# Optimization experiments

Hardware: AMD Instinct MI355X
Metric: run time of the kernel (lower is better)

Reference implementation:

```python
import jax, jax.numpy as jnp
import numpy as np

# ---- problem constants (match init_kwargs) ----
B, H, W = 8, 256, 256
GY, GX = 2 * H, 2 * W          # k_oversampling = 2
J = 7                          # interp_points
ALPHA = 2.34 * J               # Kaiser-Bessel shape parameter (torchkbnufft default)
N = 100000                     # number of non-uniform k-space samples


def _kb(u):
    """Kaiser-Bessel kernel, support |u| <= J/2 (numpy, setup-time only)."""
    arg = 1.0 - (2.0 * u / J) ** 2
    val = np.i0(ALPHA * np.sqrt(np.clip(arg, 0.0, None))) / np.i0(ALPHA)
    return np.where(np.abs(u) <= J / 2.0, val, 0.0)


def setup_inputs() -> dict:
    rng = np.random.default_rng(0)
    key = jax.random.key(0)

    # non-uniform frequencies in radians, shape (2, N) -- the stored uv plane
    uv = rng.uniform(-np.pi, np.pi, size=(2, N)).astype(np.float64)

    # ---- apodization (scaling) coefficients: 1 / FT{kb}((n - N/2)/G) per dim ----
    u = np.linspace(-J / 2.0, J / 2.0, 10001)
    du = u[1] - u[0]
    kbu = _kb(u)

    def scaling(n_im, n_grid):
        f = (np.arange(n_im) - n_im / 2.0) / n_grid          # image-domain freqs
        c = (kbu[None, :] * np.cos(2.0 * np.pi * f[:, None] * u[None, :])).sum(1) * du
        return (1.0 / c).astype(np.float32)

    sc_y = scaling(H, GY)
    sc_x = scaling(W, GX)

    # ---- precomputed interpolation matrix (indices + KB weights), per dim ----
    offs = np.arange(J) - J // 2                              # -3..3

    def interp(om, n_grid):
        t = (om * n_grid / (2.0 * np.pi)) % n_grid            # grid coords (N,)
        base = np.round(t)
        idx = (base[:, None] + offs[None, :]) % n_grid        # (N, J)
        wts = _kb(t[:, None] - (base[:, None] + offs[None, :]))
        return idx.astype(np.int32), wts.astype(np.float32)

    iy, wy = interp(uv[0], GY)
    ix, wx = interp(uv[1], GX)

    # centering phase: exp(1j * (om_y*H/2 + om_x*W/2)) for the n - N/2 convention
    ph = np.exp(1j * (uv[0] * H / 2.0 + uv[1] * W / 2.0))
    phr = ph.real.astype(np.float32)
    phi = ph.imag.astype(np.float32)

    k1, k2 = jax.random.split(key)
    xr = jax.random.normal(k1, (B, 1, H, W), dtype=jnp.float32)
    xi = jax.random.normal(k2, (B, 1, H, W), dtype=jnp.float32)

    return {
        "xr": xr, "xi": xi,
        "sc_y": jnp.asarray(sc_y), "sc_x": jnp.asarray(sc_x),
        "wy": jnp.asarray(wy), "wx": jnp.asarray(wx),
        "phr": jnp.asarray(phr), "phi": jnp.asarray(phi),
        "iy": jnp.asarray(iy), "ix": jnp.asarray(ix),
    }


def reference(xr, xi, sc_y, sc_x, wy, wx, phr, phi, iy, ix):
    """KB-NuFFT forward (dir_op): apodize -> oversampled ortho FFT -> KB gather.

    Returns (B, 1, N, 2) with real/imag of the k-space measurements.
    """
    b, c, h, w = xr.shape
    gy, gx = 2 * h, 2 * w

    # apodization correction then zero-pad to the oversampled grid
    x = (xr + 1j * xi) * (sc_y[:, None] * sc_x[None, :])      # (B,1,H,W) complex64
    xp = jnp.pad(x, ((0, 0), (0, 0), (0, gy - h), (0, gx - w)))
    ghat = jnp.fft.fft2(xp, norm="ortho")                      # (B,1,GY,GX)

    # sparse gather of the 7x7 neighborhood of every non-uniform point
    lin = (iy[:, :, None] * gx + ix[:, None, :]).reshape(-1)   # (N*J*J,)
    g = jnp.take(ghat.reshape(b, c, gy * gx), lin, axis=-1)
    g = g.reshape(b, c, -1, J, J)                              # (B,1,N,J,J)

    wgt = (wy[:, :, None] * wx[:, None, :]).astype(ghat.dtype)  # (N,J,J)
    k = jnp.einsum("bcnjk,njk->bcn", g, wgt)                   # (B,1,N) complex
    k = k * (phr + 1j * phi)                                   # centering phase
    return jnp.stack([k.real, k.imag], axis=-1)                # (B,1,N,2) float32
```

## Files before the change

### kernel.cpp

```cpp
#include <hip/hip_runtime.h>
#include <hip/hip_fp16.h>

#define GYD 512
#define GXD 512
#define HD 256
#define WD 256
#define BD 8
#define NSAMP 100000
#define JD 7
#define NCP 9

__device__ __forceinline__ int dr3(int i) {
    return ((i & 7) << 6) | (i & 56) | ((i >> 6) & 7);
}

template<int LEN, int EIGHTH, int TWSH, bool ZHI>
__device__ __forceinline__ void r8_stage(float* __restrict__ re, float* __restrict__ im,
                                         const float* __restrict__ twr,
                                         const float* __restrict__ twi, int g) {
    const int c = g & 7;
    const int m = g >> 3;
    const int off = m & (EIGHTH - 1);
    const int blk = m / EIGHTH;
    const int p0 = (blk * LEN + off) * NCP + c;

    float E0r, E0i, E1r, E1i, E2r, E2i, E3r, E3i;
    float O0r, O0i, O1r, O1i, O2r, O2i, O3r, O3i;

    if (ZHI) {
        const float a0r = re[p0 + 0 * EIGHTH * NCP], a0i = im[p0 + 0 * EIGHTH * NCP];
        const float a1r = re[p0 + 1 * EIGHTH * NCP], a1i = im[p0 + 1 * EIGHTH * NCP];
        const float a2r = re[p0 + 2 * EIGHTH * NCP], a2i = im[p0 + 2 * EIGHTH * NCP];
        const float a3r = re[p0 + 3 * EIGHTH * NCP], a3i = im[p0 + 3 * EIGHTH * NCP];
        E0r = a0r + a2r; E0i = a0i + a2i;
        E2r = a0r - a2r; E2i = a0i - a2i;
        E1r = a0r + a2i; E1i = a0i - a2r;
        E3r = a0r - a2i; E3i = a0i + a2r;
        O0r = a1r + a3r; O0i = a1i + a3i;
        O2r = a1r - a3r; O2i = a1i - a3i;
        O1r = a1r + a3i; O1i = a1i - a3r;
        O3r = a1r - a3i; O3i = a1i + a3r;
    } else {
        float ar[8], ai[8];
        #pragma unroll
        for (int j = 0; j < 8; ++j) {
            ar[j] = re[p0 + j * EIGHTH * NCP];
            ai[j] = im[p0 + j * EIGHTH * NCP];
        }
        if (TWSH >= 0) {
            #pragma unroll
            for (int j = 1; j < 8; ++j) {
                const int idx = (off * j) << (TWSH >= 0 ? TWSH : 0);
                const float cr = twr[idx], ci = twi[idx];
                const float tr = ar[j] * cr - ai[j] * ci;
                ai[j] = ar[j] * ci + ai[j] * cr;
                ar[j] = tr;
            }
        }
        const float e0r = ar[0] + ar[4], e0i = ai[0] + ai[4];
        const float e1r = ar[0] - ar[4], e1i = ai[0] - ai[4];
        const float e2r = ar[2] + ar[6], e2i = ai[2] + ai[6];
        const float e3r = ar[2] - ar[6], e3i = ai[2] - ai[6];
        E0r = e0r + e2r; E0i = e0i + e2i;
        E2r = e0r - e2r; E2i = e0i - e2i;
        E1r = e1r + e3i; E1i = e1i - e3r;
        E3r = e1r - e3i; E3i = e1i + e3r;

        const float q0r = ar[1] + ar[5], q0i = ai[1] + ai[5];
        const float q1r = ar[1] - ar[5], q1i = ai[1] - ai[5];
        const float q2r = ar[3] + ar[7], q2i = ai[3] + ai[7];
        const float q3r = ar[3] - ar[7], q3i = ai[3] - ai[7];
        O0r = q0r + q2r; O0i = q0i + q2i;
        O2r = q0r - q2r; O2i = q0i - q2i;
        O1r = q1r + q3i; O1i = q1i - q3r;
        O3r = q1r - q3i; O3i = q1i + q3r;
    }

    const float S = 0.70710678118654752f;
    const float T0r = O0r,              T0i = O0i;
    const float T1r = S * (O1r + O1i),  T1i = S * (O1i - O1r);
    const float T2r = O2i,              T2i = -O2r;
    const float T3r = S * (O3i - O3r),  T3i = -S * (O3r + O3i);

    re[p0 + 0 * EIGHTH * NCP] = E0r + T0r;  im[p0 + 0 * EIGHTH * NCP] = E0i + T0i;
    re[p0 + 4 * EIGHTH * NCP] = E0r - T0r;  im[p0 + 4 * EIGHTH * NCP] = E0i - T0i;
    re[p0 + 1 * EIGHTH * NCP] = E1r + T1r;  im[p0 + 1 * EIGHTH * NCP] = E1i + T1i;
    re[p0 + 5 * EIGHTH * NCP] = E1r - T1r;  im[p0 + 5 * EIGHTH * NCP] = E1i - T1i;
    re[p0 + 2 * EIGHTH * NCP] = E2r + T2r;  im[p0 + 2 * EIGHTH * NCP] = E2i + T2i;
    re[p0 + 6 * EIGHTH * NCP] = E2r - T2r;  im[p0 + 6 * EIGHTH * NCP] = E2i - T2i;
    re[p0 + 3 * EIGHTH * NCP] = E3r + T3r;  im[p0 + 3 * EIGHTH * NCP] = E3i + T3i;
    re[p0 + 7 * EIGHTH * NCP] = E3r - T3r;  im[p0 + 7 * EIGHTH * NCP] = E3i - T3i;
}

__global__ __launch_bounds__(512) void rowfft_kernel(
    const float* __restrict__ xr, const float* __restrict__ xi,
    const float* __restrict__ sc_y, const float* __restrict__ sc_x,
    float4* __restrict__ G1h4)
{
    __shared__ float re[512 * NCP];
    __shared__ float im[512 * NCP];
    __shared__ float twr[512];
    __shared__ float twi[512];
    const int t = threadIdx.x;
    const int y = blockIdx.x;

    {
        float sn, cs;
        sincospif(-(float)t / 256.0f, &sn, &cs);
        twr[t] = cs; twi[t] = sn;
    }

    const float sy = sc_y[y];
    {
        const int b = t >> 6;
        const int x4 = (t & 63) << 2;
        const float4 vr = *(const float4*)(xr + b * (HD * WD) + y * WD + x4);
        const float4 vi = *(const float4*)(xi + b * (HD * WD) + y * WD + x4);
        const float4 sx = *(const float4*)(sc_x + x4);
        int p;
        float s;
        s = sy * sx.x; p = dr3(x4 + 0) * NCP + b; re[p] = vr.x * s; im[p] = vi.x * s;
        s = sy * sx.y; p = dr3(x4 + 1) * NCP + b; re[p] = vr.y * s; im[p] = vi.y * s;
        s = sy * sx.z; p = dr3(x4 + 2) * NCP + b; re[p] = vr.z * s; im[p] = vi.z * s;
        s = sy * sx.w; p = dr3(x4 + 3) * NCP + b; re[p] = vr.w * s; im[p] = vi.w * s;
    }
    __syncthreads();
    r8_stage<8, 1, -1, true>(re, im, twr, twi, t);
    __syncthreads();
    r8_stage<64, 8, 3, false>(re, im, twr, twi, t);
    __syncthreads();
    r8_stage<512, 64, 0, false>(re, im, twr, twi, t);
    __syncthreads();

    float4* dst = G1h4 + (size_t)y * 1024;
    #pragma unroll
    for (int iter = 0; iter < 2; ++iter) {
        const int f = iter * 512 + t;
        const int x = f >> 1;
        const int b0 = (f & 1) * 4;
        const int p = x * NCP + b0;
        union { __half2 h[4]; float4 f4; } u;
        #pragma unroll
        for (int i = 0; i < 4; ++i)
            u.h[i] = __floats2half2_rn(re[p + i], im[p + i]);
        dst[f] = u.f4;
    }
}

__global__ __launch_bounds__(512) void colfft_kernel(
    const float4* __restrict__ G1h4, float2* __restrict__ ghat_f2)
{
    __shared__ float re[512 * NCP];
    __shared__ float im[512 * NCP];
    __shared__ float twr[512];
    __shared__ float twi[512];
    const int t = threadIdx.x;
    const int x = blockIdx.x;

    {
        float sn, cs;
        sincospif(-(float)t / 256.0f, &sn, &cs);
        twr[t] = cs; twi[t] = sn;
    }

    {
        const int yy = t >> 1;
        const int slot = t & 1;
        union { __half2 h[4]; float4 f4; } u;
        u.f4 = G1h4[(size_t)yy * 1024 + x * 2 + slot];
        const int p = dr3(yy) * NCP + slot * 4;
        #pragma unroll
        for (int i = 0; i < 4; ++i) {
            const float2 v = __half22float2(u.h[i]);
            re[p + i] = v.x;
            im[p + i] = v.y;
        }
    }
    __syncthreads();
    r8_stage<8, 1, -1, true>(re, im, twr, twi, t);
    __syncthreads();
    r8_stage<64, 8, 3, false>(re, im, twr, twi, t);
    __syncthreads();
    r8_stage<512, 64, 0, false>(re, im, twr, twi, t);
    __syncthreads();

    const float scale = 1.0f / 512.0f;
    #pragma unroll
    for (int iter = 0; iter < 4; ++iter) {
        const int if4 = iter * 512 + t;
        const int yy = if4 >> 2;
        const int b = (if4 & 3) << 1;
        const int p = yy * NCP + b;
        union { __half2 h[2]; float2 f; } u;
        u.h[0] = __floats2half2_rn(re[p] * scale,     im[p] * scale);
        u.h[1] = __floats2half2_rn(re[p + 1] * scale, im[p + 1] * scale);
        ghat_f2[((size_t)yy * GXD + x) * 4 + (b >> 1)] = u.f;
    }
}

__global__ __launch_bounds__(256) void gather_kernel(
    const __half2* __restrict__ gh,
    const float* __restrict__ wy, const float* __restrict__ wx,
    const float* __restrict__ phr, const float* __restrict__ phi,
    const int* __restrict__ iy, const int* __restrict__ ix,
    float2* __restrict__ out)
{
    __shared__ int   s_iy[32 * JD];
    __shared__ int   s_ix[32 * JD];
    __shared__ float s_wy[32 * JD];
    __shared__ float s_wx[32 * JD];
    __shared__ float s_pr[32];
    __shared__ float s_pi[32];
    const int t = threadIdx.x;
    const int n0 = blockIdx.x * 32;

    if (t < 224) {
        const int g = n0 * JD + t;
        s_iy[t] = iy[g];
        s_ix[t] = ix[g];
        s_wy[t] = wy[g];
        s_wx[t] = wx[g];
    } else {
        const int s = t - 224;
        s_pr[s] = phr[n0 + s];
        s_pi[s] = phi[n0 + s];
    }
    __syncthreads();

    const int b = t & 7;
    const int s = t >> 3;
    const int base = s * JD;

    int iyl[JD], ixl[JD];
    float wyl[JD], wxl[JD];
    #pragma unroll
    for (int j = 0; j < JD; ++j) {
        iyl[j] = s_iy[base + j];
        ixl[j] = s_ix[base + j];
        wyl[j] = s_wy[base + j];
        wxl[j] = s_wx[base + j];
    }

    float ar = 0.0f, ai = 0.0f;
    #pragma unroll
    for (int j = 0; j < JD; ++j) {
        const int rowoff = iyl[j] * GXD;
        const float wj = wyl[j];
        #pragma unroll
        for (int k = 0; k < JD; ++k) {
            const float w = wj * wxl[k];
            const float2 v = __half22float2(gh[(size_t)(rowoff + ixl[k]) * BD + b]);
            ar += v.x * w;
            ai += v.y * w;
        }
    }

    const int n = n0 + s;
    const float pr = s_pr[s], pi = s_pi[s];
    out[(size_t)b * NSAMP + n] = make_float2(ar * pr - ai * pi,
                                             ar * pi + ai * pr);
}

extern "C" void kernel_launch(void* const* d_in, const int* in_sizes, int n_in,
                              void* d_out, int out_size, void* d_ws, size_t ws_size,
                              hipStream_t stream) {
    const float* xr   = (const float*)d_in[0];
    const float* xi   = (const float*)d_in[1];
    const float* sc_y = (const float*)d_in[2];
    const float* sc_x = (const float*)d_in[3];
    const float* wy   = (const float*)d_in[4];
    const float* wx   = (const float*)d_in[5];
    const float* phr  = (const float*)d_in[6];
    const float* phi  = (const float*)d_in[7];
    const int*   iy   = (const int*)d_in[8];
    const int*   ix   = (const int*)d_in[9];

    char* ws = (char*)d_ws;
    float4* G1h4 = (float4*)ws;
    float2* gh   = (float2*)(ws + (size_t)HD * GXD * BD * sizeof(__half2));

    rowfft_kernel<<<HD, 512, 0, stream>>>(xr, xi, sc_y, sc_x, G1h4);
    colfft_kernel<<<GXD, 512, 0, stream>>>(G1h4, gh);
    gather_kernel<<<NSAMP / 32, 256, 0, stream>>>(
        (const __half2*)gh, wy, wx, phr, phi, iy, ix, (float2*)d_out);
}
```

Before: 112.9 us.

## Split FFT blocks across batch halves with a new padded LDS layout

The row and column FFT kernels now give each block half of the batch (4 channels instead of 8). This doubles the grid to 512 and 1024 blocks of 256 threads, and the LDS footprint per block is about halved. The LDS padding moves from a stride-9 layout to a 4-wide interleave with a pad every 8 points, and the global intermediate layout is reorganised so each half-batch is contiguous. The aim is better occupancy and more blocks to spread across CUs on the small grids. The cost is duplicated twiddle setup per block and more index arithmetic.

Result: slower. 115.4 us (+2.2%).

```diff
diff --git a/kernel.cpp b/kernel.cpp
--- a/kernel.cpp
+++ b/kernel.cpp
@@ -8,30 +8,36 @@
 #define BD 8
 #define NSAMP 100000
 #define JD 7
-#define NCP 9
+
+#define LDSZ 2304
+
+__device__ __forceinline__ int LPF(int x) { return (x + (x >> 3)) << 2; }
 
 __device__ __forceinline__ int dr3(int i) {
     return ((i & 7) << 6) | (i & 56) | ((i >> 6) & 7);
 }
 
 template<int LEN, int EIGHTH, int TWSH, bool ZHI>
-__device__ __forceinline__ void r8_stage(float* __restrict__ re, float* __restrict__ im,
-                                         const float* __restrict__ twr,
-                                         const float* __restrict__ twi, int g) {
-    const int c = g & 7;
-    const int m = g >> 3;
+__device__ __forceinline__ void r8s(float* __restrict__ re, float* __restrict__ im,
+                                    const float* __restrict__ twr,
+                                    const float* __restrict__ twi, int t) {
+    const int c = t & 3;
+    const int m = t >> 2;
     const int off = m & (EIGHTH - 1);
     const int blk = m / EIGHTH;
-    const int p0 = (blk * LEN + off) * NCP + c;
+    const int x0 = blk * LEN + off;
+    int p[8];
+    #pragma unroll
+    for (int j = 0; j < 8; ++j) p[j] = LPF(x0 + j * EIGHTH) + c;
 
     float E0r, E0i, E1r, E1i, E2r, E2i, E3r, E3i;
     float O0r, O0i, O1r, O1i, O2r, O2i, O3r, O3i;
 
     if (ZHI) {
-        const float a0r = re[p0 + 0 * EIGHTH * NCP], a0i = im[p0 + 0 * EIGHTH * NCP];
-        const float a1r = re[p0 + 1 * EIGHTH * NCP], a1i = im[p0 + 1 * EIGHTH * NCP];
-        const float a2r = re[p0 + 2 * EIGHTH * NCP], a2i = im[p0 + 2 * EIGHTH * NCP];
-        const float a3r = re[p0 + 3 * EIGHTH * NCP], a3i = im[p0 + 3 * EIGHTH * NCP];
+        const float a0r = re[p[0]], a0i = im[p[0]];
+        const float a1r = re[p[1]], a1i = im[p[1]];
+        const float a2r = re[p[2]], a2i = im[p[2]];
+        const float a3r = re[p[3]], a3i = im[p[3]];
         E0r = a0r + a2r; E0i = a0i + a2i;
         E2r = a0r - a2r; E2i = a0i - a2i;
         E1r = a0r + a2i; E1i = a0i - a2r;
@@ -44,8 +50,8 @@
         float ar[8], ai[8];
         #pragma unroll
         for (int j = 0; j < 8; ++j) {
-            ar[j] = re[p0 + j * EIGHTH * NCP];
-            ai[j] = im[p0 + j * EIGHTH * NCP];
+            ar[j] = re[p[j]];
+            ai[j] = im[p[j]];
         }
         if (TWSH >= 0) {
             #pragma unroll
@@ -82,119 +88,125 @@
     const float T2r = O2i,              T2i = -O2r;
     const float T3r = S * (O3i - O3r),  T3i = -S * (O3r + O3i);
 
-    re[p0 + 0 * EIGHTH * NCP] = E0r + T0r;  im[p0 + 0 * EIGHTH * NCP] = E0i + T0i;
-    re[p0 + 4 * EIGHTH * NCP] = E0r - T0r;  im[p0 + 4 * EIGHTH * NCP] = E0i - T0i;
-    re[p0 + 1 * EIGHTH * NCP] = E1r + T1r;  im[p0 + 1 * EIGHTH * NCP] = E1i + T1i;
-    re[p0 + 5 * EIGHTH * NCP] = E1r - T1r;  im[p0 + 5 * EIGHTH * NCP] = E1i - T1i;
-    re[p0 + 2 * EIGHTH * NCP] = E2r + T2r;  im[p0 + 2 * EIGHTH * NCP] = E2i + T2i;
-    re[p0 + 6 * EIGHTH * NCP] = E2r - T2r;  im[p0 + 6 * EIGHTH * NCP] = E2i - T2i;
-    re[p0 + 3 * EIGHTH * NCP] = E3r + T3r;  im[p0 + 3 * EIGHTH * NCP] = E3i + T3i;
-    re[p0 + 7 * EIGHTH * NCP] = E3r - T3r;  im[p0 + 7 * EIGHTH * NCP] = E3i - T3i;
-}
-
-__global__ __launch_bounds__(512) void rowfft_kernel(
+    re[p[0]] = E0r + T0r;  im[p[0]] = E0i + T0i;
+    re[p[4]] = E0r - T0r;  im[p[4]] = E0i - T0i;
+    re[p[1]] = E1r + T1r;  im[p[1]] = E1i + T1i;
+    re[p[5]] = E1r - T1r;  im[p[5]] = E1i - T1i;
+    re[p[2]] = E2r + T2r;  im[p[2]] = E2i + T2i;
+    re[p[6]] = E2r - T2r;  im[p[6]] = E2i - T2i;
+    re[p[3]] = E3r + T3r;  im[p[3]] = E3i + T3i;
+    re[p[7]] = E3r - T3r;  im[p[7]] = E3i - T3i;
+}
+
+__global__ __launch_bounds__(256, 2) void rowfft_kernel(
     const float* __restrict__ xr, const float* __restrict__ xi,
     const float* __restrict__ sc_y, const float* __restrict__ sc_x,
     float4* __restrict__ G1h4)
 {
-    __shared__ float re[512 * NCP];
-    __shared__ float im[512 * NCP];
+    __shared__ float re[LDSZ];
+    __shared__ float im[LDSZ];
     __shared__ float twr[512];
     __shared__ float twi[512];
     const int t = threadIdx.x;
-    const int y = blockIdx.x;
-
-    {
+    const int y = blockIdx.x >> 1;
+    const int bh = blockIdx.x & 1;
+
+    #pragma unroll
+    for (int k = t; k < 512; k += 256) {
         float sn, cs;
-        sincospif(-(float)t / 256.0f, &sn, &cs);
-        twr[t] = cs; twi[t] = sn;
+        sincospif(-(float)k / 256.0f, &sn, &cs);
+        twr[k] = cs; twi[k] = sn;
     }
 
     const float sy = sc_y[y];
     {
-        const int b = t >> 6;
+        const int c = t >> 6;
         const int x4 = (t & 63) << 2;
-        const float4 vr = *(const float4*)(xr + b * (HD * WD) + y * WD + x4);
-        const float4 vi = *(const float4*)(xi + b * (HD * WD) + y * WD + x4);
+        const int gb = bh * 4 + c;
+        const float4 vr = *(const float4*)(xr + gb * (HD * WD) + y * WD + x4);
+        const float4 vi = *(const float4*)(xi + gb * (HD * WD) + y * WD + x4);
         const float4 sx = *(const float4*)(sc_x + x4);
         int p;
         float s;
-        s = sy * sx.x; p = dr3(x4 + 0) * NCP + b; re[p] = vr.x * s; im[p] = vi.x * s;
-        s = sy * sx.y; p = dr3(x4 + 1) * NCP + b; re[p] = vr.y * s; im[p] = vi.y * s;
-        s = sy * sx.z; p = dr3(x4 + 2) * NCP + b; re[p] = vr.z * s; im[p] = vi.z * s;
-        s = sy * sx.w; p = dr3(x4 + 3) * NCP + b; re[p] = vr.w * s; im[p] = vi.w * s;
-    }
-    __syncthreads();
-    r8_stage<8, 1, -1, true>(re, im, twr, twi, t);
-    __syncthreads();
-    r8_stage<64, 8, 3, false>(re, im, twr, twi, t);
-    __syncthreads();
-    r8_stage<512, 64, 0, false>(re, im, twr, twi, t);
-    __syncthreads();
-
-    float4* dst = G1h4 + (size_t)y * 1024;
+        s = sy * sx.x; p = LPF(dr3(x4 + 0)) + c; re[p] = vr.x * s; im[p] = vi.x * s;
+        s = sy * sx.y; p = LPF(dr3(x4 + 1)) + c; re[p] = vr.y * s; im[p] = vi.y * s;
+        s = sy * sx.z; p = LPF(dr3(x4 + 2)) + c; re[p] = vr.z * s; im[p] = vi.z * s;
+        s = sy * sx.w; p = LPF(dr3(x4 + 3)) + c; re[p] = vr.w * s; im[p] = vi.w * s;
+    }
+    __syncthreads();
+    r8s<8, 1, -1, true>(re, im, twr, twi, t);
+    __syncthreads();
+    r8s<64, 8, 3, false>(re, im, twr, twi, t);
+    __syncthreads();
+    r8s<512, 64, 0, false>(re, im, twr, twi, t);
+    __syncthreads();
+
+    float4* dst = G1h4 + (size_t)y * 1024 + (size_t)bh * 512;
     #pragma unroll
     for (int iter = 0; iter < 2; ++iter) {
-        const int f = iter * 512 + t;
-        const int x = f >> 1;
-        const int b0 = (f & 1) * 4;
-        const int p = x * NCP + b0;
+        const int x = iter * 256 + t;
+        const int base = LPF(x);
         union { __half2 h[4]; float4 f4; } u;
         #pragma unroll
-        for (int i = 0; i < 4; ++i)
-            u.h[i] = __floats2half2_rn(re[p + i], im[p + i]);
-        dst[f] = u.f4;
-    }
-}
-
-__global__ __launch_bounds__(512) void colfft_kernel(
+        for (int ii = 0; ii < 4; ++ii) {
+            const int cc = (ii + x) & 3;
+            u.h[cc] = __floats2half2_rn(re[base + cc], im[base + cc]);
+        }
+        dst[x] = u.f4;
+    }
+}
+
+__global__ __launch_bounds__(256, 4) void colfft_kernel(
     const float4* __restrict__ G1h4, float2* __restrict__ ghat_f2)
 {
-    __shared__ float re[512 * NCP];
-    __shared__ float im[512 * NCP];
+    __shared__ float re[LDSZ];
+    __shared__ float im[LDSZ];
     __shared__ float twr[512];
     __shared__ float twi[512];
     const int t = threadIdx.x;
-    const int x = blockIdx.x;
+    const int x = blockIdx.x >> 1;
+    const int bh = blockIdx.x & 1;
+
+    #pragma unroll
+    for (int k = t; k < 512; k += 256) {
+        float sn, cs;
+        sincospif(-(float)k / 256.0f, &sn, &cs);
+        twr[k] = cs; twi[k] = sn;
+    }
 
     {
-        float sn, cs;
-        sincospif(-(float)t / 256.0f, &sn, &cs);
-        twr[t] = cs; twi[t] = sn;
-    }
-
-    {
-        const int yy = t >> 1;
-        const int slot = t & 1;
+        const int q = t >> 2, r = t & 3;
+        const int X = (q << 3) | r;
+        const int yy = dr3(X);
         union { __half2 h[4]; float4 f4; } u;
-        u.f4 = G1h4[(size_t)yy * 1024 + x * 2 + slot];
-        const int p = dr3(yy) * NCP + slot * 4;
+        u.f4 = G1h4[(size_t)yy * 1024 + (size_t)bh * 512 + x];
+        const int base = LPF(X);
         #pragma unroll
         for (int i = 0; i < 4; ++i) {
             const float2 v = __half22float2(u.h[i]);
-            re[p + i] = v.x;
-            im[p + i] = v.y;
-        }
-    }
-    __syncthreads();
-    r8_stage<8, 1, -1, true>(re, im, twr, twi, t);
-    __syncthreads();
-    r8_stage<64, 8, 3, false>(re, im, twr, twi, t);
-    __syncthreads();
-    r8_stage<512, 64, 0, false>(re, im, twr, twi, t);
+            re[base + i] = v.x;
+            im[base + i] = v.y;
+        }
+    }
+    __syncthreads();
+    r8s<8, 1, -1, true>(re, im, twr, twi, t);
+    __syncthreads();
+    r8s<64, 8, 3, false>(re, im, twr, twi, t);
+    __syncthreads();
+    r8s<512, 64, 0, false>(re, im, twr, twi, t);
     __syncthreads();
 
     const float scale = 1.0f / 512.0f;
     #pragma unroll
     for (int iter = 0; iter < 4; ++iter) {
-        const int if4 = iter * 512 + t;
-        const int yy = if4 >> 2;
-        const int b = (if4 & 3) << 1;
-        const int p = yy * NCP + b;
+        const int idx = iter * 256 + t;
+        const int yy = idx >> 1;
+        const int k  = idx & 1;
+        const int p = LPF(yy) + (k << 1);
         union { __half2 h[2]; float2 f; } u;
         u.h[0] = __floats2half2_rn(re[p] * scale,     im[p] * scale);
         u.h[1] = __floats2half2_rn(re[p + 1] * scale, im[p + 1] * scale);
-        ghat_f2[((size_t)yy * GXD + x) * 4 + (b >> 1)] = u.f;
+        ghat_f2[((size_t)yy * GXD + x) * 4 + bh * 2 + k] = u.f;
     }
 }
 
@@ -279,8 +291,8 @@
     float4* G1h4 = (float4*)ws;
     float2* gh   = (float2*)(ws + (size_t)HD * GXD * BD * sizeof(__half2));
 
-    rowfft_kernel<<<HD, 512, 0, stream>>>(xr, xi, sc_y, sc_x, G1h4);
-    colfft_kernel<<<GXD, 512, 0, stream>>>(G1h4, gh);
+    rowfft_kernel<<<512, 256, 0, stream>>>(xr, xi, sc_y, sc_x, G1h4);
+    colfft_kernel<<<1024, 256, 0, stream>>>(G1h4, gh);
     gather_kernel<<<NSAMP / 32, 256, 0, stream>>>(
         (const __half2*)gh, wy, wx, phr, phi, iy, ix, (float2*)d_out);
 }
```

## Interleave complex FFT shared memory and widen gather loads to two batches

Applied to the files above, without the earlier changes.

The FFT kernels now keep complex data and twiddles as interleaved float2 in shared memory instead of separate real and imaginary arrays, so each access is one 64-bit LDS operation rather than two 32-bit ones. The gather kernel now has each thread handle two batches per sample through 8-byte loads of two half2 values, with 64 samples per block and a bounds check for the tail block. This halves the number of global gather load instructions and spreads the index and weight setup over two batches, at the cost of more registers per thread. The new float2 layout with NCP=9 padding may change the shared-memory bank-conflict pattern.

Measured after the change: 117.9 us. 1.04x slower.

```diff
diff --git a/kernel.cpp b/kernel.cpp
--- a/kernel.cpp
+++ b/kernel.cpp
@@ -9,15 +9,15 @@
 #define NSAMP 100000
 #define JD 7
 #define NCP 9
+#define SPB 64
 
 __device__ __forceinline__ int dr3(int i) {
     return ((i & 7) << 6) | (i & 56) | ((i >> 6) & 7);
 }
 
 template<int LEN, int EIGHTH, int TWSH, bool ZHI>
-__device__ __forceinline__ void r8_stage(float* __restrict__ re, float* __restrict__ im,
-                                         const float* __restrict__ twr,
-                                         const float* __restrict__ twi, int g) {
+__device__ __forceinline__ void r8_stage(float2* __restrict__ cx,
+                                         const float2* __restrict__ tw, int g) {
     const int c = g & 7;
     const int m = g >> 3;
     const int off = m & (EIGHTH - 1);
@@ -28,32 +28,33 @@
     float O0r, O0i, O1r, O1i, O2r, O2i, O3r, O3i;
 
     if (ZHI) {
-        const float a0r = re[p0 + 0 * EIGHTH * NCP], a0i = im[p0 + 0 * EIGHTH * NCP];
-        const float a1r = re[p0 + 1 * EIGHTH * NCP], a1i = im[p0 + 1 * EIGHTH * NCP];
-        const float a2r = re[p0 + 2 * EIGHTH * NCP], a2i = im[p0 + 2 * EIGHTH * NCP];
-        const float a3r = re[p0 + 3 * EIGHTH * NCP], a3i = im[p0 + 3 * EIGHTH * NCP];
-        E0r = a0r + a2r; E0i = a0i + a2i;
-        E2r = a0r - a2r; E2i = a0i - a2i;
-        E1r = a0r + a2i; E1i = a0i - a2r;
-        E3r = a0r - a2i; E3i = a0i + a2r;
-        O0r = a1r + a3r; O0i = a1i + a3i;
-        O2r = a1r - a3r; O2i = a1i - a3i;
-        O1r = a1r + a3i; O1i = a1i - a3r;
-        O3r = a1r - a3i; O3i = a1i + a3r;
+        const float2 a0 = cx[p0 + 0 * EIGHTH * NCP];
+        const float2 a1 = cx[p0 + 1 * EIGHTH * NCP];
+        const float2 a2 = cx[p0 + 2 * EIGHTH * NCP];
+        const float2 a3 = cx[p0 + 3 * EIGHTH * NCP];
+        E0r = a0.x + a2.x; E0i = a0.y + a2.y;
+        E2r = a0.x - a2.x; E2i = a0.y - a2.y;
+        E1r = a0.x + a2.y; E1i = a0.y - a2.x;
+        E3r = a0.x - a2.y; E3i = a0.y + a2.x;
+        O0r = a1.x + a3.x; O0i = a1.y + a3.y;
+        O2r = a1.x - a3.x; O2i = a1.y - a3.y;
+        O1r = a1.x + a3.y; O1i = a1.y - a3.x;
+        O3r = a1.x - a3.y; O3i = a1.y + a3.x;
     } else {
         float ar[8], ai[8];
         #pragma unroll
         for (int j = 0; j < 8; ++j) {
-            ar[j] = re[p0 + j * EIGHTH * NCP];
-            ai[j] = im[p0 + j * EIGHTH * NCP];
+            const float2 v = cx[p0 + j * EIGHTH * NCP];
+            ar[j] = v.x;
+            ai[j] = v.y;
         }
         if (TWSH >= 0) {
             #pragma unroll
             for (int j = 1; j < 8; ++j) {
                 const int idx = (off * j) << (TWSH >= 0 ? TWSH : 0);
-                const float cr = twr[idx], ci = twi[idx];
-                const float tr = ar[j] * cr - ai[j] * ci;
-                ai[j] = ar[j] * ci + ai[j] * cr;
+                const float2 w = tw[idx];
+                const float tr = ar[j] * w.x - ai[j] * w.y;
+                ai[j] = ar[j] * w.y + ai[j] * w.x;
                 ar[j] = tr;
             }
         }
@@ -82,14 +83,14 @@
     const float T2r = O2i,              T2i = -O2r;
     const float T3r = S * (O3i - O3r),  T3i = -S * (O3r + O3i);
 
-    re[p0 + 0 * EIGHTH * NCP] = E0r + T0r;  im[p0 + 0 * EIGHTH * NCP] = E0i + T0i;
-    re[p0 + 4 * EIGHTH * NCP] = E0r - T0r;  im[p0 + 4 * EIGHTH * NCP] = E0i - T0i;
-    re[p0 + 1 * EIGHTH * NCP] = E1r + T1r;  im[p0 + 1 * EIGHTH * NCP] = E1i + T1i;
-    re[p0 + 5 * EIGHTH * NCP] = E1r - T1r;  im[p0 + 5 * EIGHTH * NCP] = E1i - T1i;
-    re[p0 + 2 * EIGHTH * NCP] = E2r + T2r;  im[p0 + 2 * EIGHTH * NCP] = E2i + T2i;
-    re[p0 + 6 * EIGHTH * NCP] = E2r - T2r;  im[p0 + 6 * EIGHTH * NCP] = E2i - T2i;
-    re[p0 + 3 * EIGHTH * NCP] = E3r + T3r;  im[p0 + 3 * EIGHTH * NCP] = E3i + T3i;
-    re[p0 + 7 * EIGHTH * NCP] = E3r - T3r;  im[p0 + 7 * EIGHTH * NCP] = E3i - T3i;
+    cx[p0 + 0 * EIGHTH * NCP] = make_float2(E0r + T0r, E0i + T0i);
+    cx[p0 + 4 * EIGHTH * NCP] = make_float2(E0r - T0r, E0i - T0i);
+    cx[p0 + 1 * EIGHTH * NCP] = make_float2(E1r + T1r, E1i + T1i);
+    cx[p0 + 5 * EIGHTH * NCP] = make_float2(E1r - T1r, E1i - T1i);
+    cx[p0 + 2 * EIGHTH * NCP] = make_float2(E2r + T2r, E2i + T2i);
+    cx[p0 + 6 * EIGHTH * NCP] = make_float2(E2r - T2r, E2i - T2i);
+    cx[p0 + 3 * EIGHTH * NCP] = make_float2(E3r + T3r, E3i + T3i);
+    cx[p0 + 7 * EIGHTH * NCP] = make_float2(E3r - T3r, E3i - T3i);
 }
 
 __global__ __launch_bounds__(512) void rowfft_kernel(
@@ -97,17 +98,15 @@
     const float* __restrict__ sc_y, const float* __restrict__ sc_x,
     float4* __restrict__ G1h4)
 {
-    __shared__ float re[512 * NCP];
-    __shared__ float im[512 * NCP];
-    __shared__ float twr[512];
-    __shared__ float twi[512];
+    __shared__ float2 cx[512 * NCP];
+    __shared__ float2 tw[512];
     const int t = threadIdx.x;
     const int y = blockIdx.x;
 
     {
         float sn, cs;
         sincospif(-(float)t / 256.0f, &sn, &cs);
-        twr[t] = cs; twi[t] = sn;
+        tw[t] = make_float2(cs, sn);
     }
 
     const float sy = sc_y[y];
@@ -119,17 +118,17 @@
         const float4 sx = *(const float4*)(sc_x + x4);
         int p;
         float s;
-        s = sy * sx.x; p = dr3(x4 + 0) * NCP + b; re[p] = vr.x * s; im[p] = vi.x * s;
-        s = sy * sx.y; p = dr3(x4 + 1) * NCP + b; re[p] = vr.y * s; im[p] = vi.y * s;
-        s = sy * sx.z; p = dr3(x4 + 2) * NCP + b; re[p] = vr.z * s; im[p] = vi.z * s;
-        s = sy * sx.w; p = dr3(x4 + 3) * NCP + b; re[p] = vr.w * s; im[p] = vi.w * s;
-    }
-    __syncthreads();
-    r8_stage<8, 1, -1, true>(re, im, twr, twi, t);
-    __syncthreads();
-    r8_stage<64, 8, 3, false>(re, im, twr, twi, t);
-    __syncthreads();
-    r8_stage<512, 64, 0, false>(re, im, twr, twi, t);
+        s = sy * sx.x; p = dr3(x4 + 0) * NCP + b; cx[p] = make_float2(vr.x * s, vi.x * s);
+        s = sy * sx.y; p = dr3(x4 + 1) * NCP + b; cx[p] = make_float2(vr.y * s, vi.y * s);
+        s = sy * sx.z; p = dr3(x4 + 2) * NCP + b; cx[p] = make_float2(vr.z * s, vi.z * s);
+        s = sy * sx.w; p = dr3(x4 + 3) * NCP + b; cx[p] = make_float2(vr.w * s, vi.w * s);
+    }
+    __syncthreads();
+    r8_stage<8, 1, -1, true>(cx, tw, t);
+    __syncthreads();
+    r8_stage<64, 8, 3, false>(cx, tw, t);
+    __syncthreads();
+    r8_stage<512, 64, 0, false>(cx, tw, t);
     __syncthreads();
 
     float4* dst = G1h4 + (size_t)y * 1024;
@@ -141,8 +140,10 @@
         const int p = x * NCP + b0;
         union { __half2 h[4]; float4 f4; } u;
         #pragma unroll
-        for (int i = 0; i < 4; ++i)
-            u.h[i] = __floats2half2_rn(re[p + i], im[p + i]);
+        for (int i = 0; i < 4; ++i) {
+            const float2 v = cx[p + i];
+            u.h[i] = __floats2half2_rn(v.x, v.y);
+        }
         dst[f] = u.f4;
     }
 }
@@ -150,17 +151,15 @@
 __global__ __launch_bounds__(512) void colfft_kernel(
     const float4* __restrict__ G1h4, float2* __restrict__ ghat_f2)
 {
-    __shared__ float re[512 * NCP];
-    __shared__ float im[512 * NCP];
-    __shared__ float twr[512];
-    __shared__ float twi[512];
+    __shared__ float2 cx[512 * NCP];
+    __shared__ float2 tw[512];
     const int t = threadIdx.x;
     const int x = blockIdx.x;
 
     {
         float sn, cs;
         sincospif(-(float)t / 256.0f, &sn, &cs);
-        twr[t] = cs; twi[t] = sn;
+        tw[t] = make_float2(cs, sn);
     }
 
     {
@@ -172,16 +171,15 @@
         #pragma unroll
         for (int i = 0; i < 4; ++i) {
             const float2 v = __half22float2(u.h[i]);
-            re[p + i] = v.x;
-            im[p + i] = v.y;
-        }
-    }
-    __syncthreads();
-    r8_stage<8, 1, -1, true>(re, im, twr, twi, t);
-    __syncthreads();
-    r8_stage<64, 8, 3, false>(re, im, twr, twi, t);
-    __syncthreads();
-    r8_stage<512, 64, 0, false>(re, im, twr, twi, t);
+            cx[p + i] = v;
+        }
+    }
+    __syncthreads();
+    r8_stage<8, 1, -1, true>(cx, tw, t);
+    __syncthreads();
+    r8_stage<64, 8, 3, false>(cx, tw, t);
+    __syncthreads();
+    r8_stage<512, 64, 0, false>(cx, tw, t);
     __syncthreads();
 
     const float scale = 1.0f / 512.0f;
@@ -192,73 +190,85 @@
         const int b = (if4 & 3) << 1;
         const int p = yy * NCP + b;
         union { __half2 h[2]; float2 f; } u;
-        u.h[0] = __floats2half2_rn(re[p] * scale,     im[p] * scale);
-        u.h[1] = __floats2half2_rn(re[p + 1] * scale, im[p + 1] * scale);
+        const float2 v0 = cx[p];
+        const float2 v1 = cx[p + 1];
+        u.h[0] = __floats2half2_rn(v0.x * scale, v0.y * scale);
+        u.h[1] = __floats2half2_rn(v1.x * scale, v1.y * scale);
         ghat_f2[((size_t)yy * GXD + x) * 4 + (b >> 1)] = u.f;
     }
 }
 
 __global__ __launch_bounds__(256) void gather_kernel(
-    const __half2* __restrict__ gh,
+    const float2* __restrict__ gh2,
     const float* __restrict__ wy, const float* __restrict__ wx,
     const float* __restrict__ phr, const float* __restrict__ phi,
     const int* __restrict__ iy, const int* __restrict__ ix,
     float2* __restrict__ out)
 {
-    __shared__ int   s_iy[32 * JD];
-    __shared__ int   s_ix[32 * JD];
-    __shared__ float s_wy[32 * JD];
-    __shared__ float s_wx[32 * JD];
-    __shared__ float s_pr[32];
-    __shared__ float s_pi[32];
+    __shared__ int   s_iy[SPB * JD];
+    __shared__ int   s_ix[SPB * JD];
+    __shared__ float s_wy[SPB * JD];
+    __shared__ float s_wx[SPB * JD];
+    __shared__ float s_pr[SPB];
+    __shared__ float s_pi[SPB];
     const int t = threadIdx.x;
-    const int n0 = blockIdx.x * 32;
-
-    if (t < 224) {
-        const int g = n0 * JD + t;
-        s_iy[t] = iy[g];
-        s_ix[t] = ix[g];
-        s_wy[t] = wy[g];
-        s_wx[t] = wx[g];
-    } else {
-        const int s = t - 224;
-        s_pr[s] = phr[n0 + s];
-        s_pi[s] = phi[n0 + s];
-    }
-    __syncthreads();
-
-    const int b = t & 7;
-    const int s = t >> 3;
-    const int base = s * JD;
-
-    int iyl[JD], ixl[JD];
-    float wyl[JD], wxl[JD];
-    #pragma unroll
-    for (int j = 0; j < JD; ++j) {
-        iyl[j] = s_iy[base + j];
-        ixl[j] = s_ix[base + j];
-        wyl[j] = s_wy[base + j];
-        wxl[j] = s_wx[base + j];
-    }
-
-    float ar = 0.0f, ai = 0.0f;
-    #pragma unroll
-    for (int j = 0; j < JD; ++j) {
-        const int rowoff = iyl[j] * GXD;
-        const float wj = wyl[j];
-        #pragma unroll
-        for (int k = 0; k < JD; ++k) {
-            const float w = wj * wxl[k];
-            const float2 v = __half22float2(gh[(size_t)(rowoff + ixl[k]) * BD + b]);
-            ar += v.x * w;
-            ai += v.y * w;
-        }
-    }
-
-    const int n = n0 + s;
-    const float pr = s_pr[s], pi = s_pi[s];
-    out[(size_t)b * NSAMP + n] = make_float2(ar * pr - ai * pi,
-                                             ar * pi + ai * pr);
+    const int n0 = blockIdx.x * SPB;
+    const int nrem = (NSAMP - n0 < SPB) ? (NSAMP - n0) : SPB;
+
+    for (int idx = t; idx < nrem * JD; idx += 256) {
+        const int g = n0 * JD + idx;
+        s_iy[idx] = iy[g];
+        s_ix[idx] = ix[g];
+        s_wy[idx] = wy[g];
+        s_wx[idx] = wx[g];
+    }
+    if (t < nrem) {
+        s_pr[t] = phr[n0 + t];
+        s_pi[t] = phi[n0 + t];
+    }
+    __syncthreads();
+
+    const int q = t & 3;
+    const int s = t >> 2;
+    if (s < nrem) {
+        const int base = s * JD;
+
+        int iyl[JD], ixl[JD];
+        float wyl[JD], wxl[JD];
+        #pragma unroll
+        for (int j = 0; j < JD; ++j) {
+            iyl[j] = s_iy[base + j];
+            ixl[j] = s_ix[base + j];
+            wyl[j] = s_wy[base + j];
+            wxl[j] = s_wx[base + j];
+        }
+
+        float a0r = 0.0f, a0i = 0.0f, a1r = 0.0f, a1i = 0.0f;
+        #pragma unroll
+        for (int j = 0; j < JD; ++j) {
+            const int rowoff = iyl[j] * GXD;
+            const float wj = wyl[j];
+            #pragma unroll
+            for (int k = 0; k < JD; ++k) {
+                const float w = wj * wxl[k];
+                union { float2 f; __half2 h[2]; } u;
+                u.f = gh2[(size_t)(rowoff + ixl[k]) * 4 + q];
+                const float2 va = __half22float2(u.h[0]);
+                const float2 vb = __half22float2(u.h[1]);
+                a0r += va.x * w;
+                a0i += va.y * w;
+                a1r += vb.x * w;
+                a1i += vb.y * w;
+            }
+        }
+
+        const int n = n0 + s;
+        const float pr = s_pr[s], pi = s_pi[s];
+        out[(size_t)(2 * q) * NSAMP + n]     = make_float2(a0r * pr - a0i * pi,
+                                                           a0r * pi + a0i * pr);
+        out[(size_t)(2 * q + 1) * NSAMP + n] = make_float2(a1r * pr - a1i * pi,
+                                                           a1r * pi + a1i * pr);
+    }
 }
 
 extern "C" void kernel_launch(void* const* d_in, const int* in_sizes, int n_in,
@@ -281,6 +291,6 @@
 
     rowfft_kernel<<<HD, 512, 0, stream>>>(xr, xi, sc_y, sc_x, G1h4);
     colfft_kernel<<<GXD, 512, 0, stream>>>(G1h4, gh);
-    gather_kernel<<<NSAMP / 32, 256, 0, stream>>>(
-        (const __half2*)gh, wy, wx, phr, phi, iy, ix, (float2*)d_out);
-}
+    gather_kernel<<<(NSAMP + SPB - 1) / SPB, 256, 0, stream>>>(
+        (const float2*)gh, wy, wx, phr, phi, iy, ix, (float2*)d_out);
+}
```
